# Kernel optimization log

Hardware: AMD Instinct MI355X
Metric: run time of the kernel (lower is better)

Reference implementation:

```python
import jax, jax.numpy as jnp
import numpy as np

C = 256          # channels
G = 16           # dcn groups
K = 3            # dcn kernel size (P = K*K sampling points)
PAD = 1
DIL = 1
OFFSET_SCALE = 1.0
HIDDEN = 4 * C   # mlp_ratio = 4
EPS = 1e-6


def layer_norm(x, g, b):
    mu = x.mean(-1, keepdims=True)
    var = jnp.mean((x - mu) ** 2, -1, keepdims=True)
    return (x - mu) * jax.lax.rsqrt(var + EPS) * g + b


def grid_sample_bilinear(img, grid):
    """img: (B,Cg,H,W); grid: (B,L,P,2) xy in [-1,1].
    Matches F.grid_sample(mode='bilinear', padding_mode='zeros', align_corners=False)."""
    B, Cg, H, W = img.shape
    x = (grid[..., 0] + 1.0) * (W * 0.5) - 0.5
    y = (grid[..., 1] + 1.0) * (H * 0.5) - 0.5
    x0f = jnp.floor(x); y0f = jnp.floor(y)
    wx1 = x - x0f; wy1 = y - y0f
    x0 = x0f.astype(jnp.int32); y0 = y0f.astype(jnp.int32)
    flat = img.reshape(B, Cg, H * W)

    def tap(ix, iy, w):
        valid = (ix >= 0) & (ix < W) & (iy >= 0) & (iy < H)
        idx = jnp.clip(iy, 0, H - 1) * W + jnp.clip(ix, 0, W - 1)
        v = jnp.take_along_axis(flat, idx.reshape(B, 1, -1), axis=2)
        v = v.reshape(B, Cg, idx.shape[1], idx.shape[2])
        return v * (w * valid)[:, None]

    return (tap(x0, y0, (1 - wx1) * (1 - wy1))
            + tap(x0 + 1, y0, wx1 * (1 - wy1))
            + tap(x0, y0 + 1, (1 - wx1) * wy1)
            + tap(x0 + 1, y0 + 1, wx1 * wy1))


def dcnv3(x, dw_w, dw_b, off_w, off_b, mask_w, mask_b, inp_w, inp_b, out_w, out_b):
    """DCNv3 forward (dcnv3_core_pytorch math), x: (N,H,W,C) channels_last."""
    N, H, W, Cc = x.shape
    Cg = Cc // G
    P = K * K
    xp = x @ inp_w.T + inp_b                             # input_proj
    x1 = jax.lax.conv_general_dilated(
        x, dw_w, (1, 1), [(PAD, PAD), (PAD, PAD)],
        dimension_numbers=('NHWC', 'HWIO', 'NHWC'),
        feature_group_count=Cc) + dw_b                   # depthwise conv
    off = (x1 @ off_w.T + off_b).reshape(N, H, W, G, P, 2)
    m = jax.nn.softmax((x1 @ mask_w.T + mask_b).reshape(N, H, W, G, P), axis=-1)
    Hin, Win = H + 2 * PAD, W + 2 * PAD
    xpad = jnp.pad(xp, ((0, 0), (PAD, PAD), (PAD, PAD), (0, 0)))
    base = (DIL * (K - 1)) // 2
    ry = (jnp.arange(H, dtype=x.dtype) * 1.0 + base + 0.5) / Hin
    rx = (jnp.arange(W, dtype=x.dtype) * 1.0 + base + 0.5) / Win
    ref = jnp.stack([jnp.broadcast_to(rx[None, :], (H, W)),
                     jnp.broadcast_to(ry[:, None], (H, W))], -1)   # (H,W,2) xy
    xs = (jnp.arange(K, dtype=x.dtype) * DIL - base) / Win
    ys = (jnp.arange(K, dtype=x.dtype) * DIL - base) / Hin
    gx, gy = jnp.meshgrid(xs, ys, indexing='ij')         # w-major order as in torch ref
    grid = jnp.stack([gx, gy], -1).reshape(P, 2)
    norm = jnp.array([Win, Hin], dtype=x.dtype)
    loc = (ref[None, :, :, None, None, :] + grid * OFFSET_SCALE
           + off * (OFFSET_SCALE / norm))                # (N,H,W,G,P,2)
    sg = 2.0 * loc - 1.0
    img = xpad.reshape(N, Hin, Win, G, Cg).transpose(0, 3, 4, 1, 2).reshape(N * G, Cg, Hin, Win)
    sgr = sg.transpose(0, 3, 1, 2, 4, 5).reshape(N * G, H * W, P, 2)
    sampled = grid_sample_bilinear(img, sgr)             # (N*G,Cg,HW,P)
    mr = m.transpose(0, 3, 1, 2, 4).reshape(N * G, 1, H * W, P)
    out = (sampled * mr).sum(-1).reshape(N, G, Cg, H * W)
    out = out.transpose(0, 3, 1, 2).reshape(N, H, W, Cc)
    return out @ out_w.T + out_b                         # output_proj


def setup_inputs() -> dict:
    key = jax.random.key(0)
    ks = jax.random.split(key, 10)
    N, H, W = 8, 56, 56
    P = K * K

    def rn(k, shape, s):
        return jax.random.normal(k, shape, dtype=jnp.float32) * s

    return {
        'x': jax.random.normal(ks[0], (N, H, W, C), dtype=jnp.float32),
        'ln1_g': jnp.ones((C,), jnp.float32), 'ln1_b': jnp.zeros((C,), jnp.float32),
        'dw_w': rn(ks[1], (K, K, 1, C), 0.1), 'dw_b': jnp.zeros((C,), jnp.float32),
        'off_w': rn(ks[2], (G * P * 2, C), 0.02), 'off_b': jnp.zeros((G * P * 2,), jnp.float32),
        'mask_w': rn(ks[3], (G * P, C), 0.02), 'mask_b': jnp.zeros((G * P,), jnp.float32),
        'inp_w': rn(ks[4], (C, C), 0.05), 'inp_b': jnp.zeros((C,), jnp.float32),
        'out_w': rn(ks[5], (C, C), 0.05), 'out_b': jnp.zeros((C,), jnp.float32),
        'ln2_g': jnp.ones((C,), jnp.float32), 'ln2_b': jnp.zeros((C,), jnp.float32),
        'fc1_w': rn(ks[6], (HIDDEN, C), 0.05), 'fc1_b': jnp.zeros((HIDDEN,), jnp.float32),
        'fc2_w': rn(ks[7], (C, HIDDEN), 0.05), 'fc2_b': jnp.zeros((C,), jnp.float32),
    }


def reference(x, ln1_g, ln1_b, dw_w, dw_b, off_w, off_b, mask_w, mask_b,
              inp_w, inp_b, out_w, out_b, ln2_g, ln2_b, fc1_w, fc1_b, fc2_w, fc2_b):
    # pre-norm block, no layer_scale, drop_path=0
    y = x + dcnv3(layer_norm(x, ln1_g, ln1_b), dw_w, dw_b, off_w, off_b,
                  mask_w, mask_b, inp_w, inp_b, out_w, out_b)
    h = layer_norm(y, ln2_g, ln2_b)
    h = jax.nn.gelu(h @ fc1_w.T + fc1_b, approximate=False)
    return y + (h @ fc2_w.T + fc2_b)
```

## Files before the change

### kernel.cpp

```cpp
#include <hip/hip_runtime.h>
#include <hip/hip_bf16.h>
#include <math.h>

#define NTOK 25088
#define HW_  3136
#define HH   56
#define WW   56
#define CCH  256
#define NGRP 16
#define NPTS 9
#define HIDN 1024
#define NOFFM 432
#define TPB  4

typedef __attribute__((ext_vector_type(8))) __bf16 bf16x8;
typedef __attribute__((ext_vector_type(4))) __bf16 bf16x4;
typedef __attribute__((ext_vector_type(4))) float  f32x4;

static __device__ __forceinline__ void gl_lds16(const void* g, void* l) {
    __builtin_amdgcn_global_load_lds((const __attribute__((address_space(1))) void*)g,
                                     (__attribute__((address_space(3))) void*)l, 16, 0, 0);
}

static __device__ __forceinline__ float gelu_fast(float v) {
    float z = 0.7978845608028654f * (v + 0.044715f * v * v * v);
    float t = 1.0f - 2.0f / (__expf(2.0f * z) + 1.0f);
    return 0.5f * v * (1.0f + t);
}

__global__ __launch_bounds__(256)
void cvt_all_kernel(const float* __restrict__ inp_w, const float* __restrict__ out_w,
                    const float* __restrict__ off_w, const float* __restrict__ mask_w,
                    const float* __restrict__ fc1_w, const float* __restrict__ fc2_w,
                    __bf16* wib, __bf16* wob, __bf16* wcat, __bf16* w1b, __bf16* w2b) {
    int i = blockIdx.x * 256 + threadIdx.x;
    const float* s; __bf16* d; int off;
    if (i < 16384)       { s = inp_w;  d = wib;          off = i; }
    else if (i < 32768)  { s = out_w;  d = wob;          off = i - 16384; }
    else if (i < 51200)  { s = off_w;  d = wcat;         off = i - 32768; }
    else if (i < 60416)  { s = mask_w; d = wcat + 73728; off = i - 51200; }
    else if (i < 125952) { s = fc1_w;  d = w1b;          off = i - 60416; }
    else if (i < 191488) { s = fc2_w;  d = w2b;          off = i - 125952; }
    else return;
    float4 v = ((const float4*)s)[off];
    bf16x4 o = {(__bf16)v.x, (__bf16)v.y, (__bf16)v.z, (__bf16)v.w};
    ((bf16x4*)d)[off] = o;
}

__global__ void biascat_kernel(const float* __restrict__ ob, const float* __restrict__ mb,
                               float* __restrict__ bc) {
    int i = threadIdx.x;
    if (i < 288) bc[i] = ob[i];
    else if (i < 432) bc[i] = mb[i - 288];
}

__global__ __launch_bounds__(256)
void ln_kernel(const float* __restrict__ x, const float* __restrict__ g,
               const float* __restrict__ b, __bf16* __restrict__ outb, int ntok) {
    int gid  = blockIdx.x * 256 + threadIdx.x;
    int t    = gid >> 6;
    int lane = threadIdx.x & 63;
    if (t >= ntok) return;
    float4 v = ((const float4*)(x + (size_t)t * CCH))[lane];
    float s = v.x + v.y + v.z + v.w;
#pragma unroll
    for (int o = 1; o < 64; o <<= 1) s += __shfl_xor(s, o);
    float mu = s * 0.00390625f;
    float dx = v.x - mu, dy = v.y - mu, dz = v.z - mu, dw = v.w - mu;
    float q = dx * dx + dy * dy + dz * dz + dw * dw;
#pragma unroll
    for (int o = 1; o < 64; o <<= 1) q += __shfl_xor(q, o);
    float rstd = rsqrtf(q * 0.00390625f + 1e-6f);
    float4 gg = ((const float4*)g)[lane];
    float4 bb = ((const float4*)b)[lane];
    bf16x4 ob = {(__bf16)(dx * rstd * gg.x + bb.x), (__bf16)(dy * rstd * gg.y + bb.y),
                 (__bf16)(dz * rstd * gg.z + bb.z), (__bf16)(dw * rstd * gg.w + bb.w)};
    ((bf16x4*)(outb + (size_t)t * CCH))[lane] = ob;
}

__global__ __launch_bounds__(256)
void dwconv_kernel(const __bf16* __restrict__ ln, const float* __restrict__ wt,
                   const float* __restrict__ bias, __bf16* __restrict__ out) {
    int gid = blockIdx.x * 256 + threadIdx.x;
    int t = gid >> 6;
    int cq = gid & 63;
    if (t >= NTOK) return;
    int n = t / HW_, hw = t % HW_;
    int h = hw / WW, w0 = hw % WW;
    float4 a = ((const float4*)bias)[cq];
    const bf16x4* l4 = (const bf16x4*)ln;
    const float4* w4 = (const float4*)wt;
#pragma unroll
    for (int ky = 0; ky < 3; ++ky) {
        int y = h + ky - 1;
        if (y < 0 || y >= HH) continue;
#pragma unroll
        for (int kx = 0; kx < 3; ++kx) {
            int x = w0 + kx - 1;
            if (x < 0 || x >= WW) continue;
            bf16x4 v = l4[(size_t)(n * HW_ + y * WW + x) * 64 + cq];
            float4 ww = w4[(ky * 3 + kx) * 64 + cq];
            a.x += (float)v[0] * ww.x; a.y += (float)v[1] * ww.y;
            a.z += (float)v[2] * ww.z; a.w += (float)v[3] * ww.w;
        }
    }
    bf16x4 ob = {(__bf16)a.x, (__bf16)a.y, (__bf16)a.z, (__bf16)a.w};
    ((bf16x4*)out)[(size_t)t * 64 + cq] = ob;
}

template <int EPI>
__global__ __launch_bounds__(256, 4)
void gemm_kernel(const __bf16* __restrict__ A, const __bf16* __restrict__ W,
                 const float* __restrict__ bias, const float* __restrict__ resid,
                 float* __restrict__ outf, __bf16* __restrict__ outb,
                 const int Ndim, const int Kdim) {
    __shared__ __align__(16) __bf16 Alds[2][128 * 32];
    __shared__ __align__(16) __bf16 Blds[2][128 * 32];

    const int tid  = threadIdx.x;
    const int w    = tid >> 6;
    const int lane = tid & 63;
    const int m0   = blockIdx.x * 128;
    const int n0   = blockIdx.y * 128;
    const int wr   = (w >> 1) * 64;
    const int wc   = (w & 1) * 64;

    f32x4 acc[4][4];
#pragma unroll
    for (int i = 0; i < 4; ++i)
#pragma unroll
        for (int j = 0; j < 4; ++j) acc[i][j] = (f32x4){0.f, 0.f, 0.f, 0.f};

    const int p0 = (w * 2 + 0) * 64 + lane;
    const int p1 = p0 + 64;
    const int ar0 = p0 >> 2, ab0 = ((p0 & 3) ^ ((p0 >> 4) & 3)) * 16;
    const int ar1 = p1 >> 2, ab1 = ((p1 & 3) ^ ((p1 >> 4) & 3)) * 16;
    const int br0 = p0 >> 2, br1 = p1 >> 2;
    int bR0 = n0 + ((br0 >> 6) << 6) + 4 * (br0 & 15) + ((br0 >> 4) & 3);
    int bR1 = n0 + ((br1 >> 6) << 6) + 4 * (br1 & 15) + ((br1 >> 4) & 3);
    if (bR0 > Ndim - 1) bR0 = Ndim - 1;
    if (bR1 > Ndim - 1) bR1 = Ndim - 1;
    const int bb0 = ((p0 & 3) ^ ((p0 >> 3) & 3)) * 16;
    const int bb1 = ((p1 & 3) ^ ((p1 >> 3) & 3)) * 16;

    const char* Ab = (const char*)A;
    const char* Wb = (const char*)W;
    char* AL = (char*)&Alds[0][0];
    char* BL = (char*)&Blds[0][0];
    const size_t rb = (size_t)Kdim * 2;
    const size_t sA0 = (size_t)(m0 + ar0) * rb + ab0;
    const size_t sA1 = (size_t)(m0 + ar1) * rb + ab1;
    const size_t sB0 = (size_t)bR0 * rb + bb0;
    const size_t sB1 = (size_t)bR1 * rb + bb1;
    const int d0 = (w * 2 + 0) * 1024;
    const int d1 = (w * 2 + 1) * 1024;

#define STAGE(BUF, KB)                                        \
    do {                                                      \
        gl_lds16(Ab + sA0 + (KB), AL + (BUF) * 8192 + d0);    \
        gl_lds16(Ab + sA1 + (KB), AL + (BUF) * 8192 + d1);    \
        gl_lds16(Wb + sB0 + (KB), BL + (BUF) * 8192 + d0);    \
        gl_lds16(Wb + sB1 + (KB), BL + (BUF) * 8192 + d1);    \
    } while (0)

    const int mrow = lane & 15;
    const int q    = lane >> 4;
    const int kA   = ((q ^ (mrow >> 2)) & 3) * 16;
    const int kB   = ((q ^ (mrow >> 1)) & 3) * 16;

    int cur = 0;
    STAGE(0, 0);
    __syncthreads();
    for (int k0 = 0; k0 < Kdim; k0 += 32) {
        const bool more = (k0 + 32 < Kdim);
        if (more) STAGE(cur ^ 1, (size_t)(k0 + 32) * 2);
        bf16x8 af[4], bfr[4];
#pragma unroll
        for (int i = 0; i < 4; ++i)
            af[i] = *(const bf16x8*)(AL + cur * 8192 + (wr + i * 16 + mrow) * 64 + kA);
#pragma unroll
        for (int i = 0; i < 4; ++i)
            bfr[i] = *(const bf16x8*)(BL + cur * 8192 + (wc + i * 16 + mrow) * 64 + kB);
#pragma unroll
        for (int mi = 0; mi < 4; ++mi)
#pragma unroll
            for (int ni = 0; ni < 4; ++ni)
                acc[mi][ni] = __builtin_amdgcn_mfma_f32_16x16x32_bf16(af[mi], bfr[ni], acc[mi][ni], 0, 0, 0);
        if (more) {
            __syncthreads();
            cur ^= 1;
        }
    }
#undef STAGE

    const int coll = lane & 15;
    const int rowh = (lane >> 4) * 4;
    const int col0 = n0 + wc + 4 * coll;
    if (col0 < Ndim) {
        const float4 bv = *(const float4*)(bias + col0);
#pragma unroll
        for (int mi = 0; mi < 4; ++mi) {
#pragma unroll
            for (int j = 0; j < 4; ++j) {
                const int row = m0 + wr + mi * 16 + rowh + j;
                const size_t idx = (size_t)row * (size_t)Ndim + col0;
                float4 v = make_float4(acc[mi][0][j] + bv.x, acc[mi][1][j] + bv.y,
                                       acc[mi][2][j] + bv.z, acc[mi][3][j] + bv.w);
                if (EPI == 1) {
                    const float4 r = *(const float4*)(resid + idx);
                    v.x += r.x; v.y += r.y; v.z += r.z; v.w += r.w;
                    *(float4*)(outf + idx) = v;
                } else if (EPI == 2) {
                    bf16x4 ob = {(__bf16)gelu_fast(v.x), (__bf16)gelu_fast(v.y),
                                 (__bf16)gelu_fast(v.z), (__bf16)gelu_fast(v.w)};
                    *(bf16x4*)(outb + idx) = ob;
                } else {
                    bf16x4 ob = {(__bf16)v.x, (__bf16)v.y, (__bf16)v.z, (__bf16)v.w};
                    *(bf16x4*)(outb + idx) = ob;
                }
            }
        }
    }
}

__global__ __launch_bounds__(256)
void dcn_kernel(const __bf16* __restrict__ xp, const __bf16* __restrict__ om,
                __bf16* __restrict__ out) {
    __shared__ float  raw[TPB][NOFFM];
    __shared__ int4   sidx[NPTS][TPB * NGRP];
    __shared__ float4 swt[NPTS][TPB * NGRP];
    const int tid = threadIdx.x;
    const int bid = blockIdx.x;
    const int b   = (bid & 7) * 784 + (bid >> 3);
    const int t0  = b * TPB;

    if (tid < (TPB * NOFFM) / 8) {
        bf16x8 v = *(const bf16x8*)(om + (size_t)t0 * NOFFM + tid * 8);
        float* d = &raw[0][0] + tid * 8;
#pragma unroll
        for (int k = 0; k < 8; ++k) d[k] = (float)v[k];
    }
    __syncthreads();

    if (tid < TPB * NGRP) {
        const int lt = tid >> 4, g = tid & 15;
        float* m = &raw[lt][288 + g * 9];
        float mx = m[0];
#pragma unroll
        for (int p = 1; p < 9; ++p) mx = fmaxf(mx, m[p]);
        float s = 0.f, e[9];
#pragma unroll
        for (int p = 0; p < 9; ++p) { e[p] = __expf(m[p] - mx); s += e[p]; }
        const float inv = 1.f / s;
#pragma unroll
        for (int p = 0; p < 9; ++p) m[p] = e[p] * inv;
    }
    __syncthreads();

    for (int e = tid; e < TPB * NGRP * NPTS; e += 256) {
        const int lt = e / 144, r = e % 144, g = r / 9, p = r % 9;
        const int t  = t0 + lt;
        const int hw = t % HW_;
        const int h = hw / WW, w0 = hw % WW;
        const float offx = raw[lt][g * 18 + p * 2 + 0];
        const float offy = raw[lt][g * 18 + p * 2 + 1];
        const float pm   = raw[lt][288 + g * 9 + p];
        const int kx = p / 3, ky = p % 3;
        const float fx = (float)(w0 + kx - 1) + offx;
        const float fy = (float)(h  + ky - 1) + offy;
        const float x0f = floorf(fx), y0f = floorf(fy);
        const float wx = fx - x0f, wy = fy - y0f;
        const int x0 = (int)x0f, y0 = (int)y0f;
        const bool xv0 = (unsigned)x0 < WW, xv1 = (unsigned)(x0 + 1) < WW;
        const bool yv0 = (unsigned)y0 < HH, yv1 = (unsigned)(y0 + 1) < HH;
        const int xc0 = min(max(x0, 0), WW - 1), xc1 = min(max(x0 + 1, 0), WW - 1);
        const int yc0 = min(max(y0, 0), HH - 1), yc1 = min(max(y0 + 1, 0), HH - 1);
        const int tg = lt * 16 + g;
        sidx[p][tg] = make_int4(yc0 * WW + xc0, yc0 * WW + xc1, yc1 * WW + xc0, yc1 * WW + xc1);
        swt[p][tg]  = make_float4((xv0 && yv0) ? (1.f - wx) * (1.f - wy) * pm : 0.f,
                                  (xv1 && yv0) ? wx * (1.f - wy) * pm : 0.f,
                                  (xv0 && yv1) ? (1.f - wx) * wy * pm : 0.f,
                                  (xv1 && yv1) ? wx * wy * pm : 0.f);
    }
    __syncthreads();

    const int lt = tid >> 6, lane = tid & 63;
    const int g = lane >> 2;
    const int t = t0 + lt;
    const int n = t / HW_;
    const int tg = lt * 16 + g;
    const __bf16* base = xp + (size_t)n * HW_ * CCH + lane * 4;
    f32x4 acc = {0.f, 0.f, 0.f, 0.f};
#pragma unroll
    for (int p = 0; p < NPTS; ++p) {
        const int4   id = sidx[p][tg];
        const float4 wv = swt[p][tg];
        bf16x4 v0 = *(const bf16x4*)(base + (size_t)id.x * CCH);
        bf16x4 v1 = *(const bf16x4*)(base + (size_t)id.y * CCH);
        bf16x4 v2 = *(const bf16x4*)(base + (size_t)id.z * CCH);
        bf16x4 v3 = *(const bf16x4*)(base + (size_t)id.w * CCH);
#pragma unroll
        for (int k = 0; k < 4; ++k)
            acc[k] += wv.x * (float)v0[k] + wv.y * (float)v1[k]
                    + wv.z * (float)v2[k] + wv.w * (float)v3[k];
    }
    bf16x4 ob = {(__bf16)acc[0], (__bf16)acc[1], (__bf16)acc[2], (__bf16)acc[3]};
    ((bf16x4*)out)[(size_t)t * 64 + lane] = ob;
}

extern "C" void kernel_launch(void* const* d_in, const int* in_sizes, int n_in,
                              void* d_out, int out_size, void* d_ws, size_t ws_size,
                              hipStream_t stream) {
    const float* x      = (const float*)d_in[0];
    const float* ln1_g  = (const float*)d_in[1];
    const float* ln1_b  = (const float*)d_in[2];
    const float* dw_w   = (const float*)d_in[3];
    const float* dw_b   = (const float*)d_in[4];
    const float* off_w  = (const float*)d_in[5];
    const float* off_b  = (const float*)d_in[6];
    const float* mask_w = (const float*)d_in[7];
    const float* mask_b = (const float*)d_in[8];
    const float* inp_w  = (const float*)d_in[9];
    const float* inp_b  = (const float*)d_in[10];
    const float* out_w  = (const float*)d_in[11];
    const float* out_b  = (const float*)d_in[12];
    const float* ln2_g  = (const float*)d_in[13];
    const float* ln2_b  = (const float*)d_in[14];
    const float* fc1_w  = (const float*)d_in[15];
    const float* fc1_b  = (const float*)d_in[16];
    const float* fc2_w  = (const float*)d_in[17];
    const float* fc2_b  = (const float*)d_in[18];
    float* out = (float*)d_out;

    char* ws = (char*)d_ws;
    size_t o = 0;
    auto alloc = [&](size_t bytes) { size_t r = o; o += (bytes + 255) & ~(size_t)255; return r; };
    float*  yf    = (float*)(ws + alloc((size_t)NTOK * CCH * 4));
    __bf16* x1b   = (__bf16*)(ws + alloc((size_t)NTOK * CCH * 2));
    __bf16* lnb   = (__bf16*)(ws + alloc((size_t)NTOK * CCH * 2));
    __bf16* xpb   = (__bf16*)(ws + alloc((size_t)NTOK * CCH * 2));
    __bf16* offmb = (__bf16*)(ws + alloc((size_t)NTOK * NOFFM * 2));
    alloc(4 * 1024 * 1024);
    __bf16* wib   = (__bf16*)(ws + alloc((size_t)65536 * 2));
    __bf16* wob   = (__bf16*)(ws + alloc((size_t)65536 * 2));
    __bf16* wcat  = (__bf16*)(ws + alloc((size_t)110592 * 2));
    __bf16* w1b   = (__bf16*)(ws + alloc((size_t)262144 * 2));
    __bf16* w2b   = (__bf16*)(ws + alloc((size_t)262144 * 2));
    float*  bcat  = (float*)(ws + alloc((size_t)432 * 4));
    if (ws_size < o) return;

    __bf16* dcnb = lnb;
    __bf16* l2b  = x1b;
    __bf16* h1b  = lnb;

    cvt_all_kernel<<<748, 256, 0, stream>>>(inp_w, out_w, off_w, mask_w, fc1_w, fc2_w,
                                            wib, wob, wcat, w1b, w2b);
    biascat_kernel<<<1, 512, 0, stream>>>(off_b, mask_b, bcat);

    ln_kernel<<<NTOK / 4, 256, 0, stream>>>(x, ln1_g, ln1_b, lnb, NTOK);
    dwconv_kernel<<<NTOK / 4, 256, 0, stream>>>(lnb, dw_w, dw_b, x1b);
    gemm_kernel<3><<<dim3(196, 4), 256, 0, stream>>>(x1b, wcat, bcat, nullptr, nullptr, offmb, NOFFM, 256);
    gemm_kernel<3><<<dim3(196, 2), 256, 0, stream>>>(lnb, wib, inp_b, nullptr, nullptr, xpb, 256, 256);
    dcn_kernel<<<NTOK / TPB, 256, 0, stream>>>(xpb, offmb, dcnb);
    gemm_kernel<1><<<dim3(196, 2), 256, 0, stream>>>(dcnb, wob, out_b, x, yf, nullptr, 256, 256);
    ln_kernel<<<NTOK / 4, 256, 0, stream>>>(yf, ln2_g, ln2_b, l2b, NTOK);
    gemm_kernel<2><<<dim3(196, 8), 256, 0, stream>>>(l2b, w1b, fc1_b, nullptr, nullptr, h1b, 1024, 256);
    gemm_kernel<1><<<dim3(196, 2), 256, 0, stream>>>(h1b, w2b, fc2_b, yf, out, nullptr, 256, 1024);
}
```

Measured before the change: 193.7 us.

## Shrink GEMM tiles to 64x128 with XCD-aware block remap, merge bias concat, cheaper GELU

GEMM tiles drop from 128x128 to 64x128 with a 1D grid, doubling the block count. Blocks are remapped so that consecutive tiles land on the same XCD chunk, and the launch bound rises to 6 blocks per CU to improve occupancy and wave balance on the many-CU part. The bias-concat kernel is folded into the weight-conversion kernel, removing one launch. GELU is rewritten as v*sigmoid(z) with a hardware reciprocal, which costs fewer ops. Smaller tiles reduce per-block reuse of the weight tile.

```diff
diff --git a/kernel.cpp b/kernel.cpp
--- a/kernel.cpp
+++ b/kernel.cpp
@@ -23,35 +23,35 @@
 }
 
 static __device__ __forceinline__ float gelu_fast(float v) {
-    float z = 0.7978845608028654f * (v + 0.044715f * v * v * v);
-    float t = 1.0f - 2.0f / (__expf(2.0f * z) + 1.0f);
-    return 0.5f * v * (1.0f + t);
+    float v2 = v * v;
+    float z2 = fmaf(0.0713548163f * v, v2, 1.5957691216f * v);
+    float r  = __builtin_amdgcn_rcpf(__expf(-z2) + 1.0f);
+    return v * r;
 }
 
 __global__ __launch_bounds__(256)
 void cvt_all_kernel(const float* __restrict__ inp_w, const float* __restrict__ out_w,
                     const float* __restrict__ off_w, const float* __restrict__ mask_w,
                     const float* __restrict__ fc1_w, const float* __restrict__ fc2_w,
-                    __bf16* wib, __bf16* wob, __bf16* wcat, __bf16* w1b, __bf16* w2b) {
+                    const float* __restrict__ off_b, const float* __restrict__ mask_b,
+                    __bf16* wib, __bf16* wob, __bf16* wcat, __bf16* w1b, __bf16* w2b,
+                    float* bcat) {
     int i = blockIdx.x * 256 + threadIdx.x;
+    if (i >= 191488) {
+        int j = i - 191488;
+        if (j < 432) bcat[j] = (j < 288) ? off_b[j] : mask_b[j - 288];
+        return;
+    }
     const float* s; __bf16* d; int off;
     if (i < 16384)       { s = inp_w;  d = wib;          off = i; }
     else if (i < 32768)  { s = out_w;  d = wob;          off = i - 16384; }
     else if (i < 51200)  { s = off_w;  d = wcat;         off = i - 32768; }
     else if (i < 60416)  { s = mask_w; d = wcat + 73728; off = i - 51200; }
     else if (i < 125952) { s = fc1_w;  d = w1b;          off = i - 60416; }
-    else if (i < 191488) { s = fc2_w;  d = w2b;          off = i - 125952; }
-    else return;
+    else                 { s = fc2_w;  d = w2b;          off = i - 125952; }
     float4 v = ((const float4*)s)[off];
     bf16x4 o = {(__bf16)v.x, (__bf16)v.y, (__bf16)v.z, (__bf16)v.w};
     ((bf16x4*)d)[off] = o;
-}
-
-__global__ void biascat_kernel(const float* __restrict__ ob, const float* __restrict__ mb,
-                               float* __restrict__ bc) {
-    int i = threadIdx.x;
-    if (i < 288) bc[i] = ob[i];
-    else if (i < 432) bc[i] = mb[i - 288];
 }
 
 __global__ __launch_bounds__(256)
@@ -109,58 +109,56 @@
 }
 
 template <int EPI>
-__global__ __launch_bounds__(256, 4)
+__global__ __launch_bounds__(256, 6)
 void gemm_kernel(const __bf16* __restrict__ A, const __bf16* __restrict__ W,
                  const float* __restrict__ bias, const float* __restrict__ resid,
                  float* __restrict__ outf, __bf16* __restrict__ outb,
-                 const int Ndim, const int Kdim) {
-    __shared__ __align__(16) __bf16 Alds[2][128 * 32];
+                 const int Ndim, const int Kdim, const int NB) {
+    __shared__ __align__(16) __bf16 Alds[2][64 * 32];
     __shared__ __align__(16) __bf16 Blds[2][128 * 32];
 
     const int tid  = threadIdx.x;
     const int w    = tid >> 6;
     const int lane = tid & 63;
-    const int m0   = blockIdx.x * 128;
-    const int n0   = blockIdx.y * 128;
-    const int wr   = (w >> 1) * 64;
-    const int wc   = (w & 1) * 64;
-
-    f32x4 acc[4][4];
-#pragma unroll
-    for (int i = 0; i < 4; ++i)
+    const int chunk = gridDim.x >> 3;
+    const int lin   = (blockIdx.x & 7) * chunk + (blockIdx.x >> 3);
+    const int m0 = (lin / NB) * 64;
+    const int n0 = (lin % NB) * 128;
+    const int wr = (w >> 1) * 32;
+    const int wc = (w & 1) * 64;
+
+    f32x4 acc[2][4];
+#pragma unroll
+    for (int i = 0; i < 2; ++i)
 #pragma unroll
         for (int j = 0; j < 4; ++j) acc[i][j] = (f32x4){0.f, 0.f, 0.f, 0.f};
 
-    const int p0 = (w * 2 + 0) * 64 + lane;
-    const int p1 = p0 + 64;
-    const int ar0 = p0 >> 2, ab0 = ((p0 & 3) ^ ((p0 >> 4) & 3)) * 16;
-    const int ar1 = p1 >> 2, ab1 = ((p1 & 3) ^ ((p1 >> 4) & 3)) * 16;
-    const int br0 = p0 >> 2, br1 = p1 >> 2;
+    const int pA   = tid;
+    const int arow = pA >> 2, abyte = ((pA & 3) ^ ((pA >> 4) & 3)) * 16;
+    const int pB1  = tid + 256;
+    const int br0  = tid >> 2, br1 = pB1 >> 2;
     int bR0 = n0 + ((br0 >> 6) << 6) + 4 * (br0 & 15) + ((br0 >> 4) & 3);
     int bR1 = n0 + ((br1 >> 6) << 6) + 4 * (br1 & 15) + ((br1 >> 4) & 3);
     if (bR0 > Ndim - 1) bR0 = Ndim - 1;
     if (bR1 > Ndim - 1) bR1 = Ndim - 1;
-    const int bb0 = ((p0 & 3) ^ ((p0 >> 3) & 3)) * 16;
-    const int bb1 = ((p1 & 3) ^ ((p1 >> 3) & 3)) * 16;
+    const int bb0 = ((tid & 3) ^ ((tid >> 3) & 3)) * 16;
+    const int bb1 = ((pB1 & 3) ^ ((pB1 >> 3) & 3)) * 16;
 
     const char* Ab = (const char*)A;
     const char* Wb = (const char*)W;
     char* AL = (char*)&Alds[0][0];
     char* BL = (char*)&Blds[0][0];
-    const size_t rb = (size_t)Kdim * 2;
-    const size_t sA0 = (size_t)(m0 + ar0) * rb + ab0;
-    const size_t sA1 = (size_t)(m0 + ar1) * rb + ab1;
+    const size_t rb  = (size_t)Kdim * 2;
+    const size_t sA  = (size_t)(m0 + arow) * rb + abyte;
     const size_t sB0 = (size_t)bR0 * rb + bb0;
     const size_t sB1 = (size_t)bR1 * rb + bb1;
-    const int d0 = (w * 2 + 0) * 1024;
-    const int d1 = (w * 2 + 1) * 1024;
-
-#define STAGE(BUF, KB)                                        \
-    do {                                                      \
-        gl_lds16(Ab + sA0 + (KB), AL + (BUF) * 8192 + d0);    \
-        gl_lds16(Ab + sA1 + (KB), AL + (BUF) * 8192 + d1);    \
-        gl_lds16(Wb + sB0 + (KB), BL + (BUF) * 8192 + d0);    \
-        gl_lds16(Wb + sB1 + (KB), BL + (BUF) * 8192 + d1);    \
+    const int dof = w * 1024;
+
+#define STAGE(BUF, KB)                                                 \
+    do {                                                               \
+        gl_lds16(Ab + sA  + (KB), AL + (BUF) * 4096 + dof);            \
+        gl_lds16(Wb + sB0 + (KB), BL + (BUF) * 8192 + dof);            \
+        gl_lds16(Wb + sB1 + (KB), BL + (BUF) * 8192 + 4096 + dof);     \
     } while (0)
 
     const int mrow = lane & 15;
@@ -174,15 +172,15 @@
     for (int k0 = 0; k0 < Kdim; k0 += 32) {
         const bool more = (k0 + 32 < Kdim);
         if (more) STAGE(cur ^ 1, (size_t)(k0 + 32) * 2);
-        bf16x8 af[4], bfr[4];
-#pragma unroll
-        for (int i = 0; i < 4; ++i)
-            af[i] = *(const bf16x8*)(AL + cur * 8192 + (wr + i * 16 + mrow) * 64 + kA);
+        bf16x8 af[2], bfr[4];
+#pragma unroll
+        for (int i = 0; i < 2; ++i)
+            af[i] = *(const bf16x8*)(AL + cur * 4096 + (wr + i * 16 + mrow) * 64 + kA);
 #pragma unroll
         for (int i = 0; i < 4; ++i)
             bfr[i] = *(const bf16x8*)(BL + cur * 8192 + (wc + i * 16 + mrow) * 64 + kB);
 #pragma unroll
-        for (int mi = 0; mi < 4; ++mi)
+        for (int mi = 0; mi < 2; ++mi)
 #pragma unroll
             for (int ni = 0; ni < 4; ++ni)
                 acc[mi][ni] = __builtin_amdgcn_mfma_f32_16x16x32_bf16(af[mi], bfr[ni], acc[mi][ni], 0, 0, 0);
@@ -199,7 +197,7 @@
     if (col0 < Ndim) {
         const float4 bv = *(const float4*)(bias + col0);
 #pragma unroll
-        for (int mi = 0; mi < 4; ++mi) {
+        for (int mi = 0; mi < 2; ++mi) {
 #pragma unroll
             for (int j = 0; j < 4; ++j) {
                 const int row = m0 + wr + mi * 16 + rowh + j;
@@ -353,17 +351,16 @@
     __bf16* l2b  = x1b;
     __bf16* h1b  = lnb;
 
-    cvt_all_kernel<<<748, 256, 0, stream>>>(inp_w, out_w, off_w, mask_w, fc1_w, fc2_w,
-                                            wib, wob, wcat, w1b, w2b);
-    biascat_kernel<<<1, 512, 0, stream>>>(off_b, mask_b, bcat);
+    cvt_all_kernel<<<750, 256, 0, stream>>>(inp_w, out_w, off_w, mask_w, fc1_w, fc2_w,
+                                            off_b, mask_b, wib, wob, wcat, w1b, w2b, bcat);
 
     ln_kernel<<<NTOK / 4, 256, 0, stream>>>(x, ln1_g, ln1_b, lnb, NTOK);
     dwconv_kernel<<<NTOK / 4, 256, 0, stream>>>(lnb, dw_w, dw_b, x1b);
-    gemm_kernel<3><<<dim3(196, 4), 256, 0, stream>>>(x1b, wcat, bcat, nullptr, nullptr, offmb, NOFFM, 256);
-    gemm_kernel<3><<<dim3(196, 2), 256, 0, stream>>>(lnb, wib, inp_b, nullptr, nullptr, xpb, 256, 256);
+    gemm_kernel<3><<<392 * 4, 256, 0, stream>>>(x1b, wcat, bcat, nullptr, nullptr, offmb, NOFFM, 256, 4);
+    gemm_kernel<3><<<392 * 2, 256, 0, stream>>>(lnb, wib, inp_b, nullptr, nullptr, xpb, 256, 256, 2);
     dcn_kernel<<<NTOK / TPB, 256, 0, stream>>>(xpb, offmb, dcnb);
-    gemm_kernel<1><<<dim3(196, 2), 256, 0, stream>>>(dcnb, wob, out_b, x, yf, nullptr, 256, 256);
+    gemm_kernel<1><<<392 * 2, 256, 0, stream>>>(dcnb, wob, out_b, x, yf, nullptr, 256, 256, 2);
     ln_kernel<<<NTOK / 4, 256, 0, stream>>>(yf, ln2_g, ln2_b, l2b, NTOK);
-    gemm_kernel<2><<<dim3(196, 8), 256, 0, stream>>>(l2b, w1b, fc1_b, nullptr, nullptr, h1b, 1024, 256);
-    gemm_kernel<1><<<dim3(196, 2), 256, 0, stream>>>(h1b, w2b, fc2_b, yf, out, nullptr, 256, 1024);
-}
+    gemm_kernel<2><<<392 * 8, 256, 0, stream>>>(l2b, w1b, fc1_b, nullptr, nullptr, h1b, 1024, 256, 8);
+    gemm_kernel<1><<<392 * 2, 256, 0, stream>>>(h1b, w2b, fc2_b, yf, out, nullptr, 256, 1024, 2);
+}
```

After: 183.0 us. -5.5%, faster.
